# Kernel tuning notes

Hardware: AMD Instinct MI355X
Metric: run time of the kernel (lower is better)

## Reference

```python
import jax, jax.numpy as jnp
import numpy as np

# GraphVToS (keras) faithful jax reference.
# Original math: for every atom pair (i,j), concat(vf[i], vf[j]) along features,
# project with w_vs [2F,K] + b_vs, multiply by pairwise distance vector d[i,j,c],
# sum over coordinate axis c (=3), apply activation.
# We avoid materializing the [B,N,N,3,2F] tile by splitting w_vs into the halves
# acting on vf[i] and vf[j] (exact same linear map, distributivity of concat-matmul).

B, N, C, F, K = 8, 128, 3, 64, 64

def setup_inputs() -> dict:
    key = jax.random.key(0)
    k1, k2, k3 = jax.random.split(key, 3)
    vector_features = jax.random.normal(k1, (B, N, C, F), dtype=jnp.float32)
    distances = jax.random.normal(k2, (B, N, N, C), dtype=jnp.float32)
    w_vs = jax.random.normal(k3, (2 * F, K), dtype=jnp.float32) * (1.0 / np.sqrt(2 * F))
    b_vs = jnp.zeros((K,), dtype=jnp.float32)
    return {"vector_features": vector_features, "distances": distances,
            "w_vs": w_vs, "b_vs": b_vs}

def reference(vector_features, distances, w_vs, b_vs):
    f = vector_features.shape[-1]
    w_i, w_j = w_vs[:f], w_vs[f:]          # halves acting on vf[i] / vf[j]
    # Per-atom projections: [B,N,C,K]
    p_i = jnp.einsum('bncf,fk->bnck', vector_features, w_i)
    p_j = jnp.einsum('bncf,fk->bnck', vector_features, w_j)
    # Distance-weighted reduction over coordinate axis c -> [B,N,N,K]
    s = (jnp.einsum('bick,bijc->bijk', p_i, distances)
         + jnp.einsum('bjck,bijc->bijk', p_j, distances))
    # Bias contributes b_vs * sum_c d[i,j,c]
    s = s + distances.sum(axis=-1)[..., None] * b_vs
    return jax.nn.relu(s)
```

## Files before the change

### kernel.cpp

```cpp
#include <hip/hip_runtime.h>

#define Bz 8
#define Nz 128
#define Cz 3
#define Fz 64
#define Kz 64

__global__ void proj_kernel(const float* __restrict__ vf,
                            const float* __restrict__ w,
                            float* __restrict__ P) {
    int idx = blockIdx.x * blockDim.x + threadIdx.x;
    const int PER = Bz * Nz * Cz * Kz;
    int which = idx / PER;
    int rem   = idx - which * PER;
    int k  = rem & (Kz - 1);
    int c  = (rem >> 6) % Cz;
    int bn = rem / (Cz * Kz);

    const float* vrow = vf + (bn * Cz + c) * Fz;
    const float* wcol = w + which * Fz * Kz + k;
    float acc = 0.f;
    #pragma unroll 8
    for (int f = 0; f < Fz; ++f)
        acc += vrow[f] * wcol[f * Kz];
    P[idx] = acc;
}

__global__ void pair_kernel(const float* __restrict__ d,
                            const float4* __restrict__ P4,
                            const float4* __restrict__ bvs4,
                            float4* __restrict__ out4) {
    int tid = blockIdx.x * blockDim.x + threadIdx.x;
    int k4 = tid & 15;
    int j  = (tid >> 4) & (Nz - 1);
    int i  = (tid >> 11) & (Nz - 1);
    int b  = tid >> 18;

    const float* dp = d + (((b * Nz + i) * Nz) + j) * Cz;
    float d0 = dp[0], d1 = dp[1], d2 = dp[2];
    float dsum = d0 + d1 + d2;

    const int PER4 = (Bz * Nz * Cz * Kz) / 4;
    const float4* pi = P4 + (b * Nz + i) * (Cz * Kz / 4) + k4;
    const float4* pj = P4 + PER4 + (b * Nz + j) * (Cz * Kz / 4) + k4;

    float4 a0 = pi[0],  a1 = pi[16], a2 = pi[32];
    float4 c0 = pj[0],  c1 = pj[16], c2 = pj[32];
    float4 bv = bvs4[k4];

    float4 r;
    r.x = fmaxf(d0 * (a0.x + c0.x) + d1 * (a1.x + c1.x) + d2 * (a2.x + c2.x) + dsum * bv.x, 0.f);
    r.y = fmaxf(d0 * (a0.y + c0.y) + d1 * (a1.y + c1.y) + d2 * (a2.y + c2.y) + dsum * bv.y, 0.f);
    r.z = fmaxf(d0 * (a0.z + c0.z) + d1 * (a1.z + c1.z) + d2 * (a2.z + c2.z) + dsum * bv.z, 0.f);
    r.w = fmaxf(d0 * (a0.w + c0.w) + d1 * (a1.w + c1.w) + d2 * (a2.w + c2.w) + dsum * bv.w, 0.f);
    out4[tid] = r;
}

extern "C" void kernel_launch(void* const* d_in, const int* in_sizes, int n_in,
                              void* d_out, int out_size, void* d_ws, size_t ws_size,
                              hipStream_t stream) {
    const float* vf  = (const float*)d_in[0];
    const float* dst = (const float*)d_in[1];
    const float* w   = (const float*)d_in[2];
    const float* bvs = (const float*)d_in[3];
    float* out = (float*)d_out;
    float* P   = (float*)d_ws;

    {
        int total = 2 * Bz * Nz * Cz * Kz;
        int block = 256;
        int grid = total / block;
        proj_kernel<<<grid, block, 0, stream>>>(vf, w, P);
    }
    {
        int total = Bz * Nz * Nz * Kz / 4;
        int block = 256;
        int grid = total / block;
        pair_kernel<<<grid, block, 0, stream>>>(dst, (const float4*)P,
                                                (const float4*)bvs, (float4*)out);
    }
}
```

Before: 84.56 us.

## Fold bias into projection, vectorize proj, and loop pairs per row block

The projection kernel now has each thread produce four outputs using float4 weight loads, and it adds the bias into the i-side projection. Because the bias term equals the sum over c of d_c times the bias, this folding is exact. The pair kernel now maps one block to each (b,i) row: the i-side projection is loaded once into registers and each thread loops over 8 j values, instead of every thread reloading it. This removes redundant loads and the per-pair bias work. In exchange it launches far fewer threads, which may reduce memory-level parallelism for the large output write.

```diff
diff --git a/kernel.cpp b/kernel.cpp
--- a/kernel.cpp
+++ b/kernel.cpp
@@ -6,54 +6,68 @@
 #define Fz 64
 #define Kz 64
 
-__global__ void proj_kernel(const float* __restrict__ vf,
-                            const float* __restrict__ w,
-                            float* __restrict__ P) {
+__global__ __launch_bounds__(256) void proj_kernel(const float* __restrict__ vf,
+                                                   const float4* __restrict__ w4,
+                                                   const float4* __restrict__ bv4,
+                                                   float4* __restrict__ P4) {
     int idx = blockIdx.x * blockDim.x + threadIdx.x;
-    const int PER = Bz * Nz * Cz * Kz;
-    int which = idx / PER;
-    int rem   = idx - which * PER;
-    int k  = rem & (Kz - 1);
-    int c  = (rem >> 6) % Cz;
-    int bn = rem / (Cz * Kz);
+    const int PER4 = (Bz * Nz * Cz * Kz) / 4;
+    int which = idx / PER4;
+    int rem   = idx - which * PER4;
+    int k4 = rem & 15;
+    int c  = (rem >> 4) % Cz;
+    int bn = rem / (Cz * Kz / 4);
 
-    const float* vrow = vf + (bn * Cz + c) * Fz;
-    const float* wcol = w + which * Fz * Kz + k;
-    float acc = 0.f;
+    const float*  vrow = vf + (bn * Cz + c) * Fz;
+    const float4* wcol = w4 + which * (Fz * Kz / 4) + k4;
+
+    float4 acc = make_float4(0.f, 0.f, 0.f, 0.f);
     #pragma unroll 8
-    for (int f = 0; f < Fz; ++f)
-        acc += vrow[f] * wcol[f * Kz];
-    P[idx] = acc;
+    for (int f = 0; f < Fz; ++f) {
+        float v = vrow[f];
+        float4 wv = wcol[f * 16];
+        acc.x += v * wv.x; acc.y += v * wv.y; acc.z += v * wv.z; acc.w += v * wv.w;
+    }
+    if (which == 0) {
+        float4 bv = bv4[k4];
+        acc.x += bv.x; acc.y += bv.y; acc.z += bv.z; acc.w += bv.w;
+    }
+    P4[idx] = acc;
 }
 
-__global__ void pair_kernel(const float* __restrict__ d,
-                            const float4* __restrict__ P4,
-                            const float4* __restrict__ bvs4,
-                            float4* __restrict__ out4) {
-    int tid = blockIdx.x * blockDim.x + threadIdx.x;
-    int k4 = tid & 15;
-    int j  = (tid >> 4) & (Nz - 1);
-    int i  = (tid >> 11) & (Nz - 1);
-    int b  = tid >> 18;
+__global__ __launch_bounds__(256) void pair_kernel(const float* __restrict__ d,
+                                                   const float4* __restrict__ P4,
+                                                   float4* __restrict__ out4) {
+    const int PER4 = (Bz * Nz * Cz * Kz) / 4;
+    int t   = threadIdx.x;
+    int k4  = t & 15;
+    int jc  = (t >> 4) & 15;
+    int i   = blockIdx.x & (Nz - 1);
+    int b   = blockIdx.x >> 7;
 
-    const float* dp = d + (((b * Nz + i) * Nz) + j) * Cz;
-    float d0 = dp[0], d1 = dp[1], d2 = dp[2];
-    float dsum = d0 + d1 + d2;
+    const float4* pi = P4 + (b * Nz + i) * 48 + k4;
+    float4 a0 = pi[0], a1 = pi[16], a2 = pi[32];
 
-    const int PER4 = (Bz * Nz * Cz * Kz) / 4;
-    const float4* pi = P4 + (b * Nz + i) * (Cz * Kz / 4) + k4;
-    const float4* pj = P4 + PER4 + (b * Nz + j) * (Cz * Kz / 4) + k4;
+    const float*  drow = d + ((b * Nz + i) * Nz) * Cz;
+    const float4* pjb  = P4 + PER4 + (b * Nz) * 48 + k4;
+    float4*       ob   = out4 + ((b * Nz + i) * Nz) * 16 + k4;
 
-    float4 a0 = pi[0],  a1 = pi[16], a2 = pi[32];
-    float4 c0 = pj[0],  c1 = pj[16], c2 = pj[32];
-    float4 bv = bvs4[k4];
+    #pragma unroll
+    for (int jj = 0; jj < 8; ++jj) {
+        int j = jc * 8 + jj;
+        const float* dp = drow + j * 3;
+        float d0 = dp[0], d1 = dp[1], d2 = dp[2];
 
-    float4 r;
-    r.x = fmaxf(d0 * (a0.x + c0.x) + d1 * (a1.x + c1.x) + d2 * (a2.x + c2.x) + dsum * bv.x, 0.f);
-    r.y = fmaxf(d0 * (a0.y + c0.y) + d1 * (a1.y + c1.y) + d2 * (a2.y + c2.y) + dsum * bv.y, 0.f);
-    r.z = fmaxf(d0 * (a0.z + c0.z) + d1 * (a1.z + c1.z) + d2 * (a2.z + c2.z) + dsum * bv.z, 0.f);
-    r.w = fmaxf(d0 * (a0.w + c0.w) + d1 * (a1.w + c1.w) + d2 * (a2.w + c2.w) + dsum * bv.w, 0.f);
-    out4[tid] = r;
+        const float4* pj = pjb + j * 48;
+        float4 c0 = pj[0], c1 = pj[16], c2 = pj[32];
+
+        float4 r;
+        r.x = fmaxf(d0 * (a0.x + c0.x) + d1 * (a1.x + c1.x) + d2 * (a2.x + c2.x), 0.f);
+        r.y = fmaxf(d0 * (a0.y + c0.y) + d1 * (a1.y + c1.y) + d2 * (a2.y + c2.y), 0.f);
+        r.z = fmaxf(d0 * (a0.z + c0.z) + d1 * (a1.z + c1.z) + d2 * (a2.z + c2.z), 0.f);
+        r.w = fmaxf(d0 * (a0.w + c0.w) + d1 * (a1.w + c1.w) + d2 * (a2.w + c2.w), 0.f);
+        ob[j * 16] = r;
+    }
 }
 
 extern "C" void kernel_launch(void* const* d_in, const int* in_sizes, int n_in,
@@ -66,17 +80,7 @@
     float* out = (float*)d_out;
     float* P   = (float*)d_ws;
 
-    {
-        int total = 2 * Bz * Nz * Cz * Kz;
-        int block = 256;
-        int grid = total / block;
-        proj_kernel<<<grid, block, 0, stream>>>(vf, w, P);
-    }
-    {
-        int total = Bz * Nz * Nz * Kz / 4;
-        int block = 256;
-        int grid = total / block;
-        pair_kernel<<<grid, block, 0, stream>>>(dst, (const float4*)P,
-                                                (const float4*)bvs, (float4*)out);
-    }
+    proj_kernel<<<384, 256, 0, stream>>>(vf, (const float4*)w,
+                                         (const float4*)bvs, (float4*)P);
+    pair_kernel<<<Bz * Nz, 256, 0, stream>>>(dst, (const float4*)P, (float4*)out);
 }
```

After: 79.81 us. 1.06x faster.
